# Kernel optimization log

Hardware: AMD Instinct MI355X
Metric: run time of the kernel (lower is better)

The kernel has to match this reference:

```python
import jax, jax.numpy as jnp
import numpy as np

L, D, H, T, B, V, R = 12, 1024, 16, 1024, 2, 50257, 32
HD = D // H
LORA_SCALE = 64.0 / 32.0  # alpha / rank
EPS = 1e-5


def setup_inputs() -> dict:
    key = jax.random.key(0)
    ks = iter(jax.random.split(key, 32))
    f = lambda shape, s=0.02: jax.random.normal(next(ks), shape, dtype=jnp.float32) * s
    inp = {
        'input_ids': jax.random.randint(next(ks), (B, T), 0, V, dtype=jnp.int64),
        'wte': f((V, D)), 'wpe': f((T, D)),
        'ln1_w': jnp.ones((L, D), jnp.float32), 'ln1_b': jnp.zeros((L, D), jnp.float32),
        'attn_w': f((L, 3 * D, D)), 'attn_b': jnp.zeros((L, 3 * D), jnp.float32),
        'attn_la': f((L, R, D), 0.01), 'attn_lb': f((L, 3 * D, R), 0.01),
        'proj_w': f((L, D, D)), 'proj_b': jnp.zeros((L, D), jnp.float32),
        'proj_la': f((L, R, D), 0.01), 'proj_lb': f((L, D, R), 0.01),
        'ln2_w': jnp.ones((L, D), jnp.float32), 'ln2_b': jnp.zeros((L, D), jnp.float32),
        'fc_w': f((L, 4 * D, D)), 'fc_b': jnp.zeros((L, 4 * D), jnp.float32),
        'fc_la': f((L, R, D), 0.01), 'fc_lb': f((L, 4 * D, R), 0.01),
        'mp_w': f((L, D, 4 * D)), 'mp_b': jnp.zeros((L, D), jnp.float32),
        'mp_la': f((L, R, 4 * D), 0.01), 'mp_lb': f((L, D, R), 0.01),
        'lnf_w': jnp.ones((D,), jnp.float32), 'lnf_b': jnp.zeros((D,), jnp.float32),
    }
    return inp


def _ln(x, w, b):
    m = jnp.mean(x, axis=-1, keepdims=True)
    v = jnp.mean(jnp.square(x - m), axis=-1, keepdims=True)
    return (x - m) * jax.lax.rsqrt(v + EPS) * w + b


def _lin(x, W, b, A, Bm):
    # quantized linear at 32-bit (pass-through) + LoRA: x W^T + b + scale * (x A^T) B^T
    return x @ W.T + b + ((x @ A.T) @ Bm.T) * LORA_SCALE


def _forward(input_ids, wte, wpe, ln1_w, ln1_b, attn_w, attn_b, attn_la, attn_lb,
             proj_w, proj_b, proj_la, proj_lb, ln2_w, ln2_b, fc_w, fc_b, fc_la, fc_lb,
             mp_w, mp_b, mp_la, mp_lb, lnf_w, lnf_b):
    Bq, Tq = input_ids.shape
    mask = jnp.tril(jnp.ones((Tq, Tq), dtype=bool))  # causal bias buffer
    h = wte[input_ids] + wpe[jnp.arange(Tq)]  # embed + (eval-mode) dropout

    def blk(h, p):
        l1w, l1b, aw, ab, ala, alb, pw, pb, pla, plb, l2w, l2b, fw, fb, fla, flb, mw, mb, mla, mlb = p
        x = _ln(h, l1w, l1b)
        qkv = _lin(x, aw, ab, ala, alb)  # [B,T,3D]
        q, k, v = jnp.split(qkv, 3, axis=-1)
        q = q.reshape(Bq, Tq, H, HD).transpose(0, 2, 1, 3)
        k = k.reshape(Bq, Tq, H, HD).transpose(0, 2, 1, 3)
        v = v.reshape(Bq, Tq, H, HD).transpose(0, 2, 1, 3)
        s = jnp.einsum('bhqd,bhkd->bhqk', q, k) / jnp.sqrt(jnp.float32(HD))
        s = jnp.where(mask, s, -jnp.inf)
        pa = jax.nn.softmax(s, axis=-1)
        o = jnp.einsum('bhqk,bhkd->bhqd', pa, v).transpose(0, 2, 1, 3).reshape(Bq, Tq, D)
        h = h + _lin(o, pw, pb, pla, plb)
        x = _ln(h, l2w, l2b)
        m = jax.nn.gelu(_lin(x, fw, fb, fla, flb), approximate=False)
        h = h + _lin(m, mw, mb, mla, mlb)
        return h, None

    h, _ = jax.lax.scan(blk, h, (ln1_w, ln1_b, attn_w, attn_b, attn_la, attn_lb,
                                 proj_w, proj_b, proj_la, proj_lb, ln2_w, ln2_b,
                                 fc_w, fc_b, fc_la, fc_lb, mp_w, mp_b, mp_la, mp_lb))
    return _ln(h, lnf_w, lnf_b)


def reference(input_ids, wte, wpe, ln1_w, ln1_b, attn_w, attn_b, attn_la, attn_lb,
              proj_w, proj_b, proj_la, proj_lb, ln2_w, ln2_b, fc_w, fc_b, fc_la, fc_lb,
              mp_w, mp_b, mp_la, mp_lb, lnf_w, lnf_b):
    return _forward(input_ids, wte, wpe, ln1_w, ln1_b, attn_w, attn_b, attn_la, attn_lb,
                    proj_w, proj_b, proj_la, proj_lb, ln2_w, ln2_b, fc_w, fc_b, fc_la, fc_lb,
                    mp_w, mp_b, mp_la, mp_lb, lnf_w, lnf_b)
```

## Files before the change

kernel.cpp:

```cpp
#include <hip/hip_runtime.h>
#include <math.h>

#define TT 1024
#define DD 1024
#define NH 16
#define NB 2
#define NL 12
#define RR 32
#define MM (NB * TT)

typedef __attribute__((ext_vector_type(8))) short bf16x8;
typedef __attribute__((ext_vector_type(4))) float f32x4;

__device__ __forceinline__ unsigned short f2bf(float f) {
  unsigned int u = __float_as_uint(f);
  u = (u + 0x7FFFu + ((u >> 16) & 1u)) >> 16;
  return (unsigned short)u;
}
__device__ __forceinline__ float bf2f(unsigned short u) {
  return __uint_as_float((unsigned int)u << 16);
}

typedef __attribute__((address_space(1))) void gvoid;
typedef __attribute__((address_space(3))) void lvoid;
__device__ __forceinline__ void gload_lds16(const void* g, void* l) {
  __builtin_amdgcn_global_load_lds((gvoid*)g, (lvoid*)l, 16, 0, 0);
}

__global__ __launch_bounds__(256) void embed_k(const int* __restrict__ ids,
                                               const float* __restrict__ wte,
                                               const float* __restrict__ wpe,
                                               float* __restrict__ h) {
  const int i = blockIdx.x * 256 + threadIdx.x;
  const int row = i >> 10;
  const int d = i & 1023;
  const int t = row & (TT - 1);
  const int id = ids[row];
  h[i] = wte[(size_t)id * DD + d] + wpe[(size_t)t * DD + d];
}

__global__ __launch_bounds__(256) void ln_bf_k(const float* __restrict__ x,
                                               const float* __restrict__ w,
                                               const float* __restrict__ b,
                                               unsigned short* __restrict__ out) {
  const int row = blockIdx.x;
  const float* xr = x + (size_t)row * DD;
  const float4 v = *(const float4*)(xr + threadIdx.x * 4);
  float s = v.x + v.y + v.z + v.w;
  float ss = v.x * v.x + v.y * v.y + v.z * v.z + v.w * v.w;
#pragma unroll
  for (int off = 32; off > 0; off >>= 1) {
    s += __shfl_down(s, off);
    ss += __shfl_down(ss, off);
  }
  __shared__ float rs[4], rss[4];
  const int wid = threadIdx.x >> 6;
  if ((threadIdx.x & 63) == 0) { rs[wid] = s; rss[wid] = ss; }
  __syncthreads();
  s = rs[0] + rs[1] + rs[2] + rs[3];
  ss = rss[0] + rss[1] + rss[2] + rss[3];
  const float mean = s * (1.f / DD);
  const float var = ss * (1.f / DD) - mean * mean;
  const float rstd = rsqrtf(var + 1e-5f);
  const float4 wv = *(const float4*)(w + threadIdx.x * 4);
  const float4 bv = *(const float4*)(b + threadIdx.x * 4);
  ushort4 o;
  o.x = f2bf((v.x - mean) * rstd * wv.x + bv.x);
  o.y = f2bf((v.y - mean) * rstd * wv.y + bv.y);
  o.z = f2bf((v.z - mean) * rstd * wv.z + bv.z);
  o.w = f2bf((v.w - mean) * rstd * wv.w + bv.w);
  *(ushort4*)(out + (size_t)row * DD + threadIdx.x * 4) = o;
}

__global__ __launch_bounds__(256) void ln_f_k(const float* __restrict__ x,
                                              const float* __restrict__ w,
                                              const float* __restrict__ b,
                                              float* __restrict__ out) {
  const int row = blockIdx.x;
  const float* xr = x + (size_t)row * DD;
  const float4 v = *(const float4*)(xr + threadIdx.x * 4);
  float s = v.x + v.y + v.z + v.w;
  float ss = v.x * v.x + v.y * v.y + v.z * v.z + v.w * v.w;
#pragma unroll
  for (int off = 32; off > 0; off >>= 1) {
    s += __shfl_down(s, off);
    ss += __shfl_down(ss, off);
  }
  __shared__ float rs[4], rss[4];
  const int wid = threadIdx.x >> 6;
  if ((threadIdx.x & 63) == 0) { rs[wid] = s; rss[wid] = ss; }
  __syncthreads();
  s = rs[0] + rs[1] + rs[2] + rs[3];
  ss = rss[0] + rss[1] + rss[2] + rss[3];
  const float mean = s * (1.f / DD);
  const float var = ss * (1.f / DD) - mean * mean;
  const float rstd = rsqrtf(var + 1e-5f);
  const float4 wv = *(const float4*)(w + threadIdx.x * 4);
  const float4 bv = *(const float4*)(b + threadIdx.x * 4);
  float4 o;
  o.x = (v.x - mean) * rstd * wv.x + bv.x;
  o.y = (v.y - mean) * rstd * wv.y + bv.y;
  o.z = (v.z - mean) * rstd * wv.z + bv.z;
  o.w = (v.w - mean) * rstd * wv.w + bv.w;
  *(float4*)(out + (size_t)row * DD + threadIdx.x * 4) = o;
}

__global__ __launch_bounds__(256) void cvt_lora_k(
    const float* __restrict__ ala, const float* __restrict__ alb,
    const float* __restrict__ pla, const float* __restrict__ plb,
    const float* __restrict__ fla, const float* __restrict__ flb,
    const float* __restrict__ mla, const float* __restrict__ mlb,
    unsigned short* __restrict__ out) {
  const int g = blockIdx.x * 256 + threadIdx.x;
  const int layer = g >> 19;
  const int rem = g & 524287;
  const int row = rem >> 5;
  const int r = rem & 31;
  float v;
  if (row < 1024)       v = ala[(size_t)layer * 32 * 1024 + r * 1024 + row];
  else if (row < 4096)  v = alb[(size_t)layer * 3072 * 32 + (row - 1024) * 32 + r];
  else if (row < 5120)  v = pla[(size_t)layer * 32 * 1024 + r * 1024 + (row - 4096)];
  else if (row < 6144)  v = plb[(size_t)layer * 1024 * 32 + (row - 5120) * 32 + r];
  else if (row < 7168)  v = fla[(size_t)layer * 32 * 1024 + r * 1024 + (row - 6144)];
  else if (row < 11264) v = flb[(size_t)layer * 4096 * 32 + (row - 7168) * 32 + r];
  else if (row < 15360) v = mla[(size_t)layer * 32 * 4096 + r * 4096 + (row - 11264)];
  else                  v = mlb[(size_t)layer * 1024 * 32 + (row - 15360) * 32 + r];
  out[g] = f2bf(v);
}

__global__ __launch_bounds__(256) void fusew4_k(
    const float* __restrict__ aw, const float* __restrict__ pw,
    const float* __restrict__ fw, const float* __restrict__ mw,
    const unsigned short* __restrict__ lora,
    unsigned short* __restrict__ oq, unsigned short* __restrict__ op_,
    unsigned short* __restrict__ of, unsigned short* __restrict__ om) {
  const int g = blockIdx.x;
  const int layer = g / 1536;
  const int lid = g - layer * 1536;
  const unsigned short* Lb = lora + (size_t)layer * 16384 * 32;
  const float* W;
  unsigned short* out;
  const unsigned short *Bl, *Al;
  int K, n0, kblk;
  if (lid < 384) {
    W = aw + (size_t)layer * 3 * DD * DD; out = oq + (size_t)layer * 3 * DD * DD;
    Bl = Lb + 1024 * 32; Al = Lb;
    K = DD; n0 = (lid >> 3) * 64; kblk = (lid & 7) * 128;
  } else if (lid < 512) {
    const int t = lid - 384;
    W = pw + (size_t)layer * DD * DD; out = op_ + (size_t)layer * DD * DD;
    Bl = Lb + 5120 * 32; Al = Lb + 4096 * 32;
    K = DD; n0 = (t >> 3) * 64; kblk = (t & 7) * 128;
  } else if (lid < 1024) {
    const int t = lid - 512;
    W = fw + (size_t)layer * 4 * DD * DD; out = of + (size_t)layer * 4 * DD * DD;
    Bl = Lb + 7168 * 32; Al = Lb + 6144 * 32;
    K = DD; n0 = (t >> 3) * 64; kblk = (t & 7) * 128;
  } else {
    const int t = lid - 1024;
    W = mw + (size_t)layer * DD * 4 * DD; out = om + (size_t)layer * DD * 4 * DD;
    Bl = Lb + 15360 * 32; Al = Lb + 11264 * 32;
    K = 4 * DD; n0 = (t >> 5) * 64; kblk = (t & 31) * 128;
  }
  __shared__ unsigned short dl[64 * 128];
  const int tid = threadIdx.x;
  const int w = tid >> 6, l = tid & 63;
  const int lr16 = l & 15, lg = l >> 4;
  const int nloc = w * 16 + lr16;
  const bf16x8 bfrag = *(const bf16x8*)(Bl + (size_t)(n0 + nloc) * 32 + lg * 8);
#pragma unroll
  for (int kc = 0; kc < 8; ++kc) {
    const bf16x8 afr = *(const bf16x8*)(Al + (size_t)(kblk + kc * 16 + lr16) * 32 + lg * 8);
    f32x4 acc = {};
    acc = __builtin_amdgcn_mfma_f32_16x16x32_bf16(afr, bfrag, acc, 0, 0, 0);
    ushort4 dv;
    dv.x = f2bf(2.f * acc[0]); dv.y = f2bf(2.f * acc[1]);
    dv.z = f2bf(2.f * acc[2]); dv.w = f2bf(2.f * acc[3]);
    const unsigned int byte = ((unsigned)(nloc * 256 + kc * 32 + lg * 8)) ^
                              (((unsigned)nloc & 3u) << 5);
    *(ushort4*)((char*)dl + byte) = dv;
  }
  __syncthreads();
  float4 wv[8];
#pragma unroll
  for (int it = 0; it < 8; ++it) {
    const int flat = it * 1024 + tid * 4;
    const int row = flat >> 7;
    const int k = flat & 127;
    wv[it] = *(const float4*)(W + (size_t)(n0 + row) * K + kblk + k);
  }
#pragma unroll
  for (int it = 0; it < 8; ++it) {
    const int flat = it * 1024 + tid * 4;
    const int row = flat >> 7;
    const int k = flat & 127;
    const unsigned int byte = ((unsigned)(row * 256 + k * 2)) ^
                              (((unsigned)row & 3u) << 5);
    const ushort4 dv = *(const ushort4*)((const char*)dl + byte);
    ushort4 o;
    o.x = f2bf(wv[it].x + bf2f(dv.x));
    o.y = f2bf(wv[it].y + bf2f(dv.y));
    o.z = f2bf(wv[it].z + bf2f(dv.z));
    o.w = f2bf(wv[it].w + bf2f(dv.w));
    *(ushort4*)(out + (size_t)(n0 + row) * K + kblk + k) = o;
  }
}

template <int BMt, int BNt, int BKt, int MODE>
__global__ __launch_bounds__(256) void gemm_t(const unsigned short* __restrict__ A,
                                              const unsigned short* __restrict__ Wt,
                                              const float* __restrict__ bias,
                                              const float* __restrict__ res,
                                              float* __restrict__ Cf,
                                              unsigned short* __restrict__ Cb,
                                              unsigned short* __restrict__ vt,
                                              int M, int N, int K) {
  constexpr int MI2 = BMt / 32, NJ2 = BNt / 32;
  constexpr int SB = BKt * 2;
  constexpr int SL = BKt / 8;
  constexpr int RC = 1024 / SB;
  constexpr int CAw = BMt / RC / 4;
  constexpr int CBw = BNt / RC / 4;
  __shared__ unsigned short As[BMt * BKt];
  __shared__ unsigned short Bs[BNt * BKt];
  const int tid = threadIdx.x;
  const int w = tid >> 6, l = tid & 63;
  const int gx = gridDim.x;
  const int bid = blockIdx.y * gx + blockIdx.x;
  const int cpx = (gx * gridDim.y) >> 3;
  const int logical = (bid & 7) * cpx + (bid >> 3);
  const int bm = (logical / gx) * BMt, bn = (logical % gx) * BNt;
  const int wr = w >> 1, wc = w & 1;
  const int lr16 = l & 15, lg = l >> 4, l7 = l & 7;
  const int rin = l / SL;
  const int slot = l % SL;
  f32x4 acc[MI2][NJ2] = {};
  for (int k0 = 0; k0 < K; k0 += BKt) {
    __syncthreads();
#pragma unroll
    for (int i = 0; i < CAw; ++i) {
      const int ch = w * CAw + i;
      const int row = ch * RC + rin;
      gload_lds16(A + (size_t)(bm + row) * K + k0 + ((slot ^ (row & 7)) * 8),
                  (char*)As + ch * 1024);
    }
#pragma unroll
    for (int i = 0; i < CBw; ++i) {
      const int ch = w * CBw + i;
      const int row = ch * RC + rin;
      gload_lds16(Wt + (size_t)(bn + row) * K + k0 + ((slot ^ (row & 7)) * 8),
                  (char*)Bs + ch * 1024);
    }
    __syncthreads();
#pragma unroll
    for (int kk = 0; kk < BKt / 32; ++kk) {
      bf16x8 af[MI2], bfr[NJ2];
      const int q = (kk * 4 + lg) ^ l7;
#pragma unroll
      for (int mi = 0; mi < MI2; ++mi)
        af[mi] = *(const bf16x8*)((const char*)As +
            (wr * (BMt / 2) + mi * 16 + lr16) * SB + q * 16);
#pragma unroll
      for (int nj = 0; nj < NJ2; ++nj)
        bfr[nj] = *(const bf16x8*)((const char*)Bs +
            (wc * (BNt / 2) + nj * 16 + lr16) * SB + q * 16);
#pragma unroll
      for (int mi = 0; mi < MI2; ++mi)
#pragma unroll
        for (int nj = 0; nj < NJ2; ++nj)
          acc[mi][nj] = __builtin_amdgcn_mfma_f32_16x16x32_bf16(
              af[mi], bfr[nj], acc[mi][nj], 0, 0, 0);
    }
  }
  const int cr = lg * 4;
  const int cc = lr16;
#pragma unroll
  for (int mi = 0; mi < MI2; ++mi) {
    const int gr0 = bm + wr * (BMt / 2) + mi * 16 + cr;
#pragma unroll
    for (int nj = 0; nj < NJ2; ++nj) {
      const int gc = bn + wc * (BNt / 2) + nj * 16 + cc;
      const float bv = bias[gc];
      if (MODE == 3) {
        if (gc < 2048) {
#pragma unroll
          for (int r = 0; r < 4; ++r)
            Cb[(size_t)(gr0 + r) * 2048 + gc] = f2bf(acc[mi][nj][r] + bv);
        } else {
          const int hv = gc - 2048;
          const int b_ = gr0 >> 10, t0 = gr0 & 1023;
          ushort4 u;
          u.x = f2bf(acc[mi][nj][0] + bv); u.y = f2bf(acc[mi][nj][1] + bv);
          u.z = f2bf(acc[mi][nj][2] + bv); u.w = f2bf(acc[mi][nj][3] + bv);
          *(ushort4*)(vt + ((size_t)(b_ * 1024 + hv)) * 1024 + t0) = u;
        }
      } else if (MODE == 1) {
#pragma unroll
        for (int r = 0; r < 4; ++r) {
          const size_t idx = (size_t)(gr0 + r) * N + gc;
          Cf[idx] = acc[mi][nj][r] + bv + res[idx];
        }
      } else {
#pragma unroll
        for (int r = 0; r < 4; ++r) {
          float v = acc[mi][nj][r] + bv;
          v = 0.5f * v * (1.f + erff(v * 0.70710678118654752f));
          Cb[(size_t)(gr0 + r) * N + gc] = f2bf(v);
        }
      }
    }
  }
}

#define SM_SCALE_LOG2E 0.18033688011112042f
__global__ __launch_bounds__(256) void attn3_k(const unsigned short* __restrict__ qk,
                                               const unsigned short* __restrict__ vt,
                                               unsigned short* __restrict__ out) {
  const int qt = 15 - blockIdx.x;
  const int bh = blockIdx.y;
  const int b = bh >> 4, hh = bh & 15;
  const int tid = threadIdx.x;
  const int w = tid >> 6, l = tid & 63;
  const int lg = l >> 4;
  const int lr = l & 15;

  __shared__ unsigned short Kt[2][64 * 64];
  __shared__ unsigned short Vb[2][64 * 64];
  __shared__ unsigned short Pb[4][16 * 64];

  bf16x8 qf[2];
  {
    const unsigned short* qp =
        qk + ((size_t)(b * TT + qt * 64 + w * 16 + lr)) * 2048 + hh * 64 + lg * 8;
    qf[0] = *(const bf16x8*)(qp);
    qf[1] = *(const bf16x8*)(qp + 32);
  }
  f32x4 oacc[4] = {};
  float mrow[4] = {-1e30f, -1e30f, -1e30f, -1e30f};
  float lrow[4] = {0.f, 0.f, 0.f, 0.f};

  auto stage = [&](int buf, int kt) {
#pragma unroll
    for (int oo = 0; oo < 2; ++oo) {
      const int o = w + oo * 4;
      const int row = o * 8 + (l >> 3);
      const int sc = ((l & 7) ^ (l >> 3)) * 8;
      const unsigned short* ks =
          qk + ((size_t)(b * TT + kt * 64 + row)) * 2048 + 1024 + hh * 64 + sc;
      gload_lds16(ks, (char*)&Kt[buf][0] + o * 1024);
      const unsigned short* vs =
          vt + ((size_t)(bh * 64 + row)) * 1024 + kt * 64 + sc;
      gload_lds16(vs, (char*)&Vb[buf][0] + o * 1024);
    }
  };

  stage(0, 0);
  int cur = 0;
  unsigned short* Pw = &Pb[w][0];
  const int qlocal = w * 16 + lg * 4;

  for (int kt = 0; kt <= qt; ++kt) {
    __syncthreads();
    if (kt < qt) stage(cur ^ 1, kt + 1);
    const unsigned short* Kb_ = &Kt[cur][0];
    const unsigned short* Vb_ = &Vb[cur][0];
    const int effc = lr & 7;

    f32x4 s[4];
#pragma unroll
    for (int j = 0; j < 4; ++j) {
      f32x4 sj = {};
#pragma unroll
      for (int ks = 0; ks < 2; ++ks) {
        const bf16x8 kf = *(const bf16x8*)((const char*)Kb_ + (j * 16 + lr) * 128 +
                                           (((ks * 4 + lg) ^ effc) * 16));
        sj = __builtin_amdgcn_mfma_f32_16x16x32_bf16(qf[ks], kf, sj, 0, 0, 0);
      }
      s[j] = sj;
    }

    const bool last = (kt == qt);
    float tv[4][4];
#pragma unroll
    for (int j = 0; j < 4; ++j)
#pragma unroll
      for (int r = 0; r < 4; ++r) {
        float v = s[j][r] * SM_SCALE_LOG2E;
        if (last && (j * 16 + lr > qlocal + r)) v = -1e30f;
        tv[j][r] = v;
      }
    float corr[4];
#pragma unroll
    for (int r = 0; r < 4; ++r) {
      float mx = fmaxf(fmaxf(tv[0][r], tv[1][r]), fmaxf(tv[2][r], tv[3][r]));
      mx = fmaxf(mx, __shfl_xor(mx, 1));
      mx = fmaxf(mx, __shfl_xor(mx, 2));
      mx = fmaxf(mx, __shfl_xor(mx, 4));
      mx = fmaxf(mx, __shfl_xor(mx, 8));
      const float mn = fmaxf(mrow[r], mx);
      corr[r] = exp2f(mrow[r] - mn);
      mrow[r] = mn;
      lrow[r] *= corr[r];
    }
#pragma unroll
    for (int dt = 0; dt < 4; ++dt) {
      oacc[dt][0] *= corr[0]; oacc[dt][1] *= corr[1];
      oacc[dt][2] *= corr[2]; oacc[dt][3] *= corr[3];
    }
#pragma unroll
    for (int j = 0; j < 4; ++j)
#pragma unroll
      for (int r = 0; r < 4; ++r) {
        const float p = exp2f(tv[j][r] - mrow[r]);
        lrow[r] += p;
        const int q = lg * 4 + r;
        const int kv = j * 16 + lr;
        *(unsigned short*)((char*)Pw + q * 128 + ((kv * 2) ^ ((q & 7) << 4))) = f2bf(p);
      }
    asm volatile("s_waitcnt lgkmcnt(0)" ::: "memory");
    __builtin_amdgcn_sched_barrier(0);

#pragma unroll
    for (int ks = 0; ks < 2; ++ks) {
      const bf16x8 pf = *(const bf16x8*)((const char*)Pw + lr * 128 +
                                         (((ks * 4 + lg) ^ effc) * 16));
#pragma unroll
      for (int dt = 0; dt < 4; ++dt) {
        const bf16x8 vf = *(const bf16x8*)((const char*)Vb_ + (dt * 16 + lr) * 128 +
                                           (((ks * 4 + lg) ^ effc) * 16));
        oacc[dt] = __builtin_amdgcn_mfma_f32_16x16x32_bf16(pf, vf, oacc[dt], 0, 0, 0);
      }
    }
    cur ^= 1;
  }

#pragma unroll
  for (int r = 0; r < 4; ++r) {
    float lv = lrow[r];
    lv += __shfl_xor(lv, 1);
    lv += __shfl_xor(lv, 2);
    lv += __shfl_xor(lv, 4);
    lv += __shfl_xor(lv, 8);
    lrow[r] = 1.f / lv;
  }
  unsigned short* ob = out + ((size_t)(b * TT + qt * 64 + w * 16 + lg * 4)) * 1024 + hh * 64 + lr;
#pragma unroll
  for (int r = 0; r < 4; ++r)
#pragma unroll
    for (int dt = 0; dt < 4; ++dt)
      ob[(size_t)r * 1024 + dt * 16] = f2bf(oacc[dt][r] * lrow[r]);
}

extern "C" void kernel_launch(void* const* d_in, const int* in_sizes, int n_in,
                              void* d_out, int out_size, void* d_ws, size_t ws_size,
                              hipStream_t stream) {
  (void)in_sizes; (void)n_in; (void)out_size; (void)ws_size;
  const int* ids = (const int*)d_in[0];
  const float* wte = (const float*)d_in[1];
  const float* wpe = (const float*)d_in[2];
  const float* ln1w = (const float*)d_in[3];
  const float* ln1b = (const float*)d_in[4];
  const float* attnw = (const float*)d_in[5];
  const float* attnb = (const float*)d_in[6];
  const float* attnla = (const float*)d_in[7];
  const float* attnlb = (const float*)d_in[8];
  const float* projw = (const float*)d_in[9];
  const float* projb = (const float*)d_in[10];
  const float* projla = (const float*)d_in[11];
  const float* projlb = (const float*)d_in[12];
  const float* ln2w = (const float*)d_in[13];
  const float* ln2b = (const float*)d_in[14];
  const float* fcw = (const float*)d_in[15];
  const float* fcb = (const float*)d_in[16];
  const float* fcla = (const float*)d_in[17];
  const float* fclb = (const float*)d_in[18];
  const float* mpw = (const float*)d_in[19];
  const float* mpb = (const float*)d_in[20];
  const float* mpla = (const float*)d_in[21];
  const float* mplb = (const float*)d_in[22];
  const float* lnfw = (const float*)d_in[23];
  const float* lnfb = (const float*)d_in[24];

  char* ws = (char*)d_ws;
  float* h = (float*)ws;                        ws += (size_t)MM * DD * 4;
  unsigned short* x = (unsigned short*)ws;      ws += (size_t)MM * DD * 2;
  unsigned short* qkb = (unsigned short*)ws;    ws += (size_t)MM * 2 * DD * 2;
  unsigned short* vtb = (unsigned short*)ws;    ws += (size_t)MM * DD * 2;
  unsigned short* ho = (unsigned short*)ws;     ws += (size_t)MM * DD * 2;
  unsigned short* hm = (unsigned short*)ws;     ws += (size_t)MM * 4 * DD * 2;
  unsigned short* wqkvA = (unsigned short*)ws;  ws += (size_t)NL * 3 * DD * DD * 2;
  unsigned short* wprojA = (unsigned short*)ws; ws += (size_t)NL * DD * DD * 2;
  unsigned short* wfcA = (unsigned short*)ws;   ws += (size_t)NL * 4 * DD * DD * 2;
  unsigned short* wmpA = (unsigned short*)ws;   ws += (size_t)NL * DD * 4 * DD * 2;
  unsigned short* loraP = (unsigned short*)ws;  ws += (size_t)NL * 16384 * 32 * 2;

  hipLaunchKernelGGL(embed_k, dim3(MM * DD / 256), dim3(256), 0, stream, ids, wte, wpe, h);

  hipLaunchKernelGGL(cvt_lora_k, dim3(NL * 16384 * 32 / 256), dim3(256), 0, stream,
                     attnla, attnlb, projla, projlb, fcla, fclb, mpla, mplb, loraP);
  hipLaunchKernelGGL(fusew4_k, dim3(NL * 1536), dim3(256), 0, stream,
                     attnw, projw, fcw, mpw, loraP, wqkvA, wprojA, wfcA, wmpA);

  for (int l = 0; l < NL; ++l) {
    const float* ab = attnb + (size_t)l * 3 * DD;
    const float* pb = projb + (size_t)l * DD;
    const float* fb = fcb + (size_t)l * 4 * DD;
    const float* mb = mpb + (size_t)l * DD;
    const unsigned short* wqkv = wqkvA + (size_t)l * 3 * DD * DD;
    const unsigned short* wproj = wprojA + (size_t)l * DD * DD;
    const unsigned short* wfc = wfcA + (size_t)l * 4 * DD * DD;
    const unsigned short* wmp = wmpA + (size_t)l * DD * 4 * DD;

    hipLaunchKernelGGL(ln_bf_k, dim3(MM), dim3(256), 0, stream, h,
                       ln1w + (size_t)l * DD, ln1b + (size_t)l * DD, x);
    hipLaunchKernelGGL((gemm_t<128, 64, 128, 3>), dim3(3 * DD / 64, MM / 128), dim3(256), 0,
                       stream, x, wqkv, ab, (const float*)nullptr, (float*)nullptr,
                       qkb, vtb, MM, 3 * DD, DD);
    hipLaunchKernelGGL(attn3_k, dim3(TT / 64, NB * NH), dim3(256), 0, stream, qkb, vtb, ho);
    hipLaunchKernelGGL((gemm_t<64, 64, 128, 1>), dim3(DD / 64, MM / 64), dim3(256), 0,
                       stream, ho, wproj, pb, h, h, (unsigned short*)nullptr,
                       (unsigned short*)nullptr, MM, DD, DD);
    hipLaunchKernelGGL(ln_bf_k, dim3(MM), dim3(256), 0, stream, h,
                       ln2w + (size_t)l * DD, ln2b + (size_t)l * DD, x);
    hipLaunchKernelGGL((gemm_t<128, 64, 64, 2>), dim3(4 * DD / 64, MM / 128), dim3(256), 0,
                       stream, x, wfc, fb, (const float*)nullptr, (float*)nullptr, hm,
                       (unsigned short*)nullptr, MM, 4 * DD, DD);
    hipLaunchKernelGGL((gemm_t<64, 64, 128, 1>), dim3(DD / 64, MM / 64), dim3(256), 0,
                       stream, hm, wmp, mb, h, h, (unsigned short*)nullptr,
                       (unsigned short*)nullptr, MM, DD, 4 * DD);
  }

  hipLaunchKernelGGL(ln_f_k, dim3(MM), dim3(256), 0, stream, h, lnfw, lnfb, (float*)d_out);
}
```

Before: 2.003 ms.

## Fuse LoRA into weights per layer inside the loop using one reused buffer

```diff
diff --git a/kernel.cpp b/kernel.cpp
--- a/kernel.cpp
+++ b/kernel.cpp
@@ -128,38 +128,31 @@
   out[g] = f2bf(v);
 }
 
-__global__ __launch_bounds__(256) void fusew4_k(
+__global__ __launch_bounds__(256) void fusew5_k(
     const float* __restrict__ aw, const float* __restrict__ pw,
     const float* __restrict__ fw, const float* __restrict__ mw,
-    const unsigned short* __restrict__ lora,
+    const unsigned short* __restrict__ Lb,
     unsigned short* __restrict__ oq, unsigned short* __restrict__ op_,
     unsigned short* __restrict__ of, unsigned short* __restrict__ om) {
-  const int g = blockIdx.x;
-  const int layer = g / 1536;
-  const int lid = g - layer * 1536;
-  const unsigned short* Lb = lora + (size_t)layer * 16384 * 32;
+  const int lid = blockIdx.x;
   const float* W;
   unsigned short* out;
   const unsigned short *Bl, *Al;
   int K, n0, kblk;
   if (lid < 384) {
-    W = aw + (size_t)layer * 3 * DD * DD; out = oq + (size_t)layer * 3 * DD * DD;
-    Bl = Lb + 1024 * 32; Al = Lb;
+    W = aw; out = oq; Bl = Lb + 1024 * 32; Al = Lb;
     K = DD; n0 = (lid >> 3) * 64; kblk = (lid & 7) * 128;
   } else if (lid < 512) {
     const int t = lid - 384;
-    W = pw + (size_t)layer * DD * DD; out = op_ + (size_t)layer * DD * DD;
-    Bl = Lb + 5120 * 32; Al = Lb + 4096 * 32;
+    W = pw; out = op_; Bl = Lb + 5120 * 32; Al = Lb + 4096 * 32;
     K = DD; n0 = (t >> 3) * 64; kblk = (t & 7) * 128;
   } else if (lid < 1024) {
     const int t = lid - 512;
-    W = fw + (size_t)layer * 4 * DD * DD; out = of + (size_t)layer * 4 * DD * DD;
-    Bl = Lb + 7168 * 32; Al = Lb + 6144 * 32;
+    W = fw; out = of; Bl = Lb + 7168 * 32; Al = Lb + 6144 * 32;
     K = DD; n0 = (t >> 3) * 64; kblk = (t & 7) * 128;
   } else {
     const int t = lid - 1024;
-    W = mw + (size_t)layer * DD * 4 * DD; out = om + (size_t)layer * DD * 4 * DD;
-    Bl = Lb + 15360 * 32; Al = Lb + 11264 * 32;
+    W = mw; out = om; Bl = Lb + 15360 * 32; Al = Lb + 11264 * 32;
     K = 4 * DD; n0 = (t >> 5) * 64; kblk = (t & 31) * 128;
   }
   __shared__ unsigned short dl[64 * 128];
@@ -189,6 +182,7 @@
     const int k = flat & 127;
     wv[it] = *(const float4*)(W + (size_t)(n0 + row) * K + kblk + k);
   }
+  asm volatile("s_waitcnt vmcnt(0)" ::: "memory");
 #pragma unroll
   for (int it = 0; it < 8; ++it) {
     const int flat = it * 1024 + tid * 4;
@@ -488,28 +482,27 @@
   unsigned short* vtb = (unsigned short*)ws;    ws += (size_t)MM * DD * 2;
   unsigned short* ho = (unsigned short*)ws;     ws += (size_t)MM * DD * 2;
   unsigned short* hm = (unsigned short*)ws;     ws += (size_t)MM * 4 * DD * 2;
-  unsigned short* wqkvA = (unsigned short*)ws;  ws += (size_t)NL * 3 * DD * DD * 2;
-  unsigned short* wprojA = (unsigned short*)ws; ws += (size_t)NL * DD * DD * 2;
-  unsigned short* wfcA = (unsigned short*)ws;   ws += (size_t)NL * 4 * DD * DD * 2;
-  unsigned short* wmpA = (unsigned short*)ws;   ws += (size_t)NL * DD * 4 * DD * 2;
+  unsigned short* wqkv = (unsigned short*)ws;   ws += (size_t)3 * DD * DD * 2;
+  unsigned short* wproj = (unsigned short*)ws;  ws += (size_t)DD * DD * 2;
+  unsigned short* wfc = (unsigned short*)ws;    ws += (size_t)4 * DD * DD * 2;
+  unsigned short* wmp = (unsigned short*)ws;    ws += (size_t)DD * 4 * DD * 2;
   unsigned short* loraP = (unsigned short*)ws;  ws += (size_t)NL * 16384 * 32 * 2;
 
   hipLaunchKernelGGL(embed_k, dim3(MM * DD / 256), dim3(256), 0, stream, ids, wte, wpe, h);
 
   hipLaunchKernelGGL(cvt_lora_k, dim3(NL * 16384 * 32 / 256), dim3(256), 0, stream,
                      attnla, attnlb, projla, projlb, fcla, fclb, mpla, mplb, loraP);
-  hipLaunchKernelGGL(fusew4_k, dim3(NL * 1536), dim3(256), 0, stream,
-                     attnw, projw, fcw, mpw, loraP, wqkvA, wprojA, wfcA, wmpA);
 
   for (int l = 0; l < NL; ++l) {
     const float* ab = attnb + (size_t)l * 3 * DD;
     const float* pb = projb + (size_t)l * DD;
     const float* fb = fcb + (size_t)l * 4 * DD;
     const float* mb = mpb + (size_t)l * DD;
-    const unsigned short* wqkv = wqkvA + (size_t)l * 3 * DD * DD;
-    const unsigned short* wproj = wprojA + (size_t)l * DD * DD;
-    const unsigned short* wfc = wfcA + (size_t)l * 4 * DD * DD;
-    const unsigned short* wmp = wmpA + (size_t)l * DD * 4 * DD;
+
+    hipLaunchKernelGGL(fusew5_k, dim3(1536), dim3(256), 0, stream,
+                       attnw + (size_t)l * 3 * DD * DD, projw + (size_t)l * DD * DD,
+                       fcw + (size_t)l * 4 * DD * DD, mpw + (size_t)l * DD * 4 * DD,
+                       loraP + (size_t)l * 16384 * 32, wqkv, wproj, wfc, wmp);
 
     hipLaunchKernelGGL(ln_bf_k, dim3(MM), dim3(256), 0, stream, h,
                        ln1w + (size_t)l * DD, ln1b + (size_t)l * DD, x);
```

Measured after the change: 1.868 ms. 6.8% less time.
